# Optimization experiments

Hardware: AMD Instinct MI355X
Metric: run time of the kernel (lower is better)

Reference implementation:

```python
import jax, jax.numpy as jnp
import numpy as np
import math

L, N, D = 1024, 64, 64
O = 1024

def setup_inputs() -> dict:
    key = jax.random.key(0)
    k1, k2 = jax.random.split(key)
    x = jax.random.normal(k1, (L, N, D), dtype=jnp.float32)
    upfold = jax.random.normal(k2, (O, N, D), dtype=jnp.float32)
    return {"x": x, "upfold": upfold}

def reference(x, upfold):
    # x: [L, N, D], upfold: [O, N, D]
    d = x.shape[-1]
    scale = 1.0 / math.sqrt(d)
    # affinities: [L, O, N]
    affinities = jnp.einsum('lnd,ond->lon', x, upfold) * scale
    # weighted sum with (sigmoid - 0.5) weights: [L, N, D]
    features = jnp.einsum('lon,ond->lnd', jax.nn.sigmoid(affinities) - 0.5, upfold)
    return features
```

## Files before the change

### kernel.cpp

```cpp
#include <hip/hip_runtime.h>
#include <stdint.h>

#define L_DIM 1024
#define N_DIM 64
#define D_DIM 64
#define O_DIM 1024
#define ND    4096
#define NT    16

typedef float    floatx16 __attribute__((ext_vector_type(16)));
typedef _Float16 half8    __attribute__((ext_vector_type(8)));
typedef _Float16 h2       __attribute__((ext_vector_type(2)));
typedef __fp16   fp16x2   __attribute__((ext_vector_type(2)));

#define BUF_STRIDE 17920

__device__ __forceinline__ uint32_t pkh2(float a, float b) {
    fp16x2 p = __builtin_amdgcn_cvt_pkrtz(a, b);
    return __builtin_bit_cast(uint32_t, p);
}

__device__ __forceinline__ half8 mk_frag(uint32_t a, uint32_t b, uint32_t c, uint32_t d) {
    union { uint32_t u[4]; half8 v; } U;
    U.u[0] = a; U.u[1] = b; U.u[2] = c; U.u[3] = d;
    return U.v;
}

__device__ __forceinline__ uint32_t psig(float s0, float s1) {
    const h2 HI = {(_Float16)41.6f,        (_Float16)41.6f};
    const h2 LO = {(_Float16)-41.6f,       (_Float16)-41.6f};
    const h2 SC = {(_Float16)0.0625f,      (_Float16)0.0625f};
    const h2 C0 = {(_Float16)0.03099238f,  (_Float16)0.03099238f};
    const h2 C1 = {(_Float16)-0.00842090f, (_Float16)-0.00842090f};
    const h2 C2 = {(_Float16)0.00151845f,  (_Float16)0.00151845f};
    const h2 C3 = {(_Float16)-1.02197e-4f, (_Float16)-1.02197e-4f};
    h2 s = __builtin_bit_cast(h2, pkh2(s0, s1));
    s = __builtin_elementwise_min(s, HI);
    s = __builtin_elementwise_max(s, LO);
    h2 ha = s * SC;
    h2 v  = ha * ha;
    h2 w  = C2 + v * C3;
    w     = C1 + v * w;
    w     = C0 + v * w;
    h2 f  = s * w;
    return __builtin_bit_cast(uint32_t, f);
}

__device__ __forceinline__ void load_tile(const float* ubase, int ot,
                                          int r8, int c, float4* va, float4* vb) {
    const float* pr = ubase + (size_t)(ot * 64 + 2 * r8) * ND + 4 * c;
    #pragma unroll
    for (int j = 0; j < 2; ++j) {
        va[j] = *(const float4*)(pr + (size_t)(32 * j) * ND);
        vb[j] = *(const float4*)(pr + (size_t)(32 * j) * ND + ND);
    }
}

__global__ void __launch_bounds__(256, 2)
corr_kernel(const float* __restrict__ x, const float* __restrict__ up,
            float* __restrict__ out)
{
    __shared__ __align__(16) unsigned char smem[2 * BUF_STRIDE];

    const int tid  = threadIdx.x;
    const int lane = tid & 63;
    const int wid  = tid >> 6;
    const int l31  = lane & 31;
    const int h    = lane >> 5;
    const int r8   = tid >> 4;
    const int c    = tid & 15;
    const int n    = blockIdx.x;
    const int lb   = blockIdx.y;
    const int lw   = lb * 128 + wid * 32 + l31;

    const float* ubase = up + (size_t)n * D_DIM;

    float4 va[2], vb[2];
    load_tile(ubase, 0, r8, c, va, vb);

    half8 Xf[4];
    {
        float (*Xs)[68] = (float (*)[68])smem;
        const int xr = tid >> 1;
        const int xh = tid & 1;
        const float* xsrc = x + (size_t)(lb * 128 + xr) * ND + n * D_DIM;
        #pragma unroll
        for (int j = 0; j < 8; ++j) {
            const int f4i = xh * 8 + j;
            *(float4*)&Xs[xr][4 * f4i] = *(const float4*)(xsrc + 4 * f4i);
        }
        __syncthreads();
        const int rl = wid * 32 + l31;
        #pragma unroll
        for (int kk = 0; kk < 4; ++kk) {
            float4 f1 = *(const float4*)&Xs[rl][16 * kk + 8 * h];
            float4 f2 = *(const float4*)&Xs[rl][16 * kk + 8 * h + 4];
            Xf[kk] = mk_frag(pkh2(f1.x, f1.y), pkh2(f1.z, f1.w),
                             pkh2(f2.x, f2.y), pkh2(f2.z, f2.w));
        }
        __syncthreads();
    }

    #pragma unroll
    for (int j = 0; j < 2; ++j) {
        uint16_t (*Ub)[72]  = (uint16_t (*)[72])(smem);
        uint32_t (*Ut2)[68] = (uint32_t (*)[68])(smem + 9216);
        *(uint2*)&Ub[2*r8 + 32*j][4*c] =
            make_uint2(pkh2(va[j].x, va[j].y), pkh2(va[j].z, va[j].w));
        *(uint2*)&Ub[2*r8 + 32*j + 1][4*c] =
            make_uint2(pkh2(vb[j].x, vb[j].y), pkh2(vb[j].z, vb[j].w));
        *(uint4*)&Ut2[r8 + 16*j][4*c] =
            make_uint4(pkh2(va[j].x, vb[j].x), pkh2(va[j].y, vb[j].y),
                       pkh2(va[j].z, vb[j].z), pkh2(va[j].w, vb[j].w));
    }
    load_tile(ubase, 1, r8, c, va, vb);
    __syncthreads();

    floatx16 F0, F1;
    #pragma unroll
    for (int i = 0; i < 16; ++i) { F0[i] = 0.0f; F1[i] = 0.0f; }

    for (int ot = 0; ot < NT; ++ot) {
        const int b = ot & 1;
        uint16_t (*Ub)[72]   = (uint16_t (*)[72])(smem + b * BUF_STRIDE);
        const uint32_t* utp  = (const uint32_t*)(smem + b * BUF_STRIDE + 9216);
        uint16_t (*Ubn)[72]  = (uint16_t (*)[72])(smem + (b ^ 1) * BUF_STRIDE);
        uint32_t (*Ut2n)[68] = (uint32_t (*)[68])(smem + (b ^ 1) * BUF_STRIDE + 9216);

        half8 A0k[4], A1k[4];
        #pragma unroll
        for (int kk = 0; kk < 4; ++kk) {
            A0k[kk] = *(const half8*)&Ub[l31][16 * kk + 8 * h];
            A1k[kk] = *(const half8*)&Ub[32 + l31][16 * kk + 8 * h];
        }

        if (ot + 1 < NT) {
            #pragma unroll
            for (int j = 0; j < 2; ++j) {
                *(uint2*)&Ubn[2*r8 + 32*j][4*c] =
                    make_uint2(pkh2(va[j].x, va[j].y), pkh2(va[j].z, va[j].w));
                *(uint2*)&Ubn[2*r8 + 32*j + 1][4*c] =
                    make_uint2(pkh2(vb[j].x, vb[j].y), pkh2(vb[j].z, vb[j].w));
                *(uint4*)&Ut2n[r8 + 16*j][4*c] =
                    make_uint4(pkh2(va[j].x, vb[j].x), pkh2(va[j].y, vb[j].y),
                               pkh2(va[j].z, vb[j].z), pkh2(va[j].w, vb[j].w));
            }
        }
        if (ot + 2 < NT)
            load_tile(ubase, ot + 2, r8, c, va, vb);

        floatx16 S0, S1;
        #pragma unroll
        for (int i = 0; i < 16; ++i) { S0[i] = 0.0f; S1[i] = 0.0f; }
        #pragma unroll
        for (int kk = 0; kk < 4; ++kk) {
            S0 = __builtin_amdgcn_mfma_f32_32x32x16_f16(A0k[kk], Xf[kk], S0, 0, 0, 0);
            S1 = __builtin_amdgcn_mfma_f32_32x32x16_f16(A1k[kk], Xf[kk], S1, 0, 0, 0);
        }

        uint32_t P[16];
        #pragma unroll
        for (int m = 0; m < 8; ++m) P[m]     = psig(S0[2*m], S0[2*m+1]);
        #pragma unroll
        for (int m = 0; m < 8; ++m) P[8 + m] = psig(S1[2*m], S1[2*m+1]);

        uint32_t R[8];
        #pragma unroll
        for (int c2 = 0; c2 < 4; ++c2) {
            const uint32_t* Q = P + (c2 >> 1) * 8;
            const int t4 = (c2 & 1) * 4;
            R[2*c2]   = __shfl_xor(h ? Q[t4]     : Q[t4 + 2], 32);
            R[2*c2+1] = __shfl_xor(h ? Q[t4 + 1] : Q[t4 + 3], 32);
        }
        #pragma unroll
        for (int c2 = 0; c2 < 4; ++c2) {
            const uint32_t* Q = P + (c2 >> 1) * 8;
            const int t4 = (c2 & 1) * 4;
            half8 B = h ? mk_frag(R[2*c2], R[2*c2+1], Q[t4 + 2], Q[t4 + 3])
                        : mk_frag(Q[t4], Q[t4 + 1], R[2*c2], R[2*c2+1]);
            const int opb = 8 * c2 + 4 * h;
            uint32_t a0[4], a1[4];
            #pragma unroll
            for (int k = 0; k < 4; ++k) {
                a0[k] = utp[(opb + k) * 68 + l31];
                a1[k] = utp[(opb + k) * 68 + 32 + l31];
            }
            half8 A0 = mk_frag(a0[0], a0[1], a0[2], a0[3]);
            half8 A1 = mk_frag(a1[0], a1[1], a1[2], a1[3]);
            F0 = __builtin_amdgcn_mfma_f32_32x32x16_f16(A0, B, F0, 0, 0, 0);
            F1 = __builtin_amdgcn_mfma_f32_32x32x16_f16(A1, B, F1, 0, 0, 0);
        }
        __syncthreads();
    }

    float* op = out + (size_t)lw * ND + n * D_DIM;
    #pragma unroll
    for (int q = 0; q < 4; ++q) {
        float4 a; a.x = F0[4*q]; a.y = F0[4*q+1]; a.z = F0[4*q+2]; a.w = F0[4*q+3];
        *(float4*)(op + 8*q + 4*h) = a;
        float4 bq; bq.x = F1[4*q]; bq.y = F1[4*q+1]; bq.z = F1[4*q+2]; bq.w = F1[4*q+3];
        *(float4*)(op + 32 + 8*q + 4*h) = bq;
    }
}

extern "C" void kernel_launch(void* const* d_in, const int* in_sizes, int n_in,
                              void* d_out, int out_size, void* d_ws, size_t ws_size,
                              hipStream_t stream)
{
    const float* x  = (const float*)d_in[0];
    const float* up = (const float*)d_in[1];
    float* out      = (float*)d_out;
    dim3 grid(N_DIM, L_DIM / 128);
    corr_kernel<<<grid, dim3(256), 0, stream>>>(x, up, out);
}
```

Before: 101.2 us.

## Precompute fp16 upfold layouts in a prepass and stream them via direct global-to-LDS loads

A new prepass kernel converts upfold to fp16 once, writing both a row-major and a transposed layout into workspace. The main kernel then stages tiles straight into LDS with global_load_lds and XOR-swizzled addressing, so it no longer does per-tile fp32 loads, conversion and LDS writes in registers. Each of the eight L-blocks previously repeated that conversion for the same n. The cost is a second kernel launch and an extra workspace round trip through global memory, and the prefetch of the next tile now overlaps the current tile's compute without a register-held copy.

```diff
diff --git a/kernel.cpp b/kernel.cpp
--- a/kernel.cpp
+++ b/kernel.cpp
@@ -1,19 +1,16 @@
 #include <hip/hip_runtime.h>
 #include <stdint.h>
 
-#define L_DIM 1024
-#define N_DIM 64
-#define D_DIM 64
-#define O_DIM 1024
-#define ND    4096
-#define NT    16
+#define ND       4096
+#define NT       16
+#define A_OFF    0
+#define B_OFF    8388608
+#define N_STRIDE 131072
 
 typedef float    floatx16 __attribute__((ext_vector_type(16)));
 typedef _Float16 half8    __attribute__((ext_vector_type(8)));
 typedef _Float16 h2       __attribute__((ext_vector_type(2)));
 typedef __fp16   fp16x2   __attribute__((ext_vector_type(2)));
-
-#define BUF_STRIDE 17920
 
 __device__ __forceinline__ uint32_t pkh2(float a, float b) {
     fp16x2 p = __builtin_amdgcn_cvt_pkrtz(a, b);
@@ -46,44 +43,81 @@
     return __builtin_bit_cast(uint32_t, f);
 }
 
-__device__ __forceinline__ void load_tile(const float* ubase, int ot,
-                                          int r8, int c, float4* va, float4* vb) {
-    const float* pr = ubase + (size_t)(ot * 64 + 2 * r8) * ND + 4 * c;
+__device__ __forceinline__ void gl_lds16(const void* g, void* l) {
+    __builtin_amdgcn_global_load_lds(
+        (const __attribute__((address_space(1))) unsigned int*)g,
+        (__attribute__((address_space(3))) unsigned int*)l, 16, 0, 0);
+}
+
+__global__ void __launch_bounds__(256, 4)
+conv_kernel(const float* __restrict__ up, uint8_t* __restrict__ ws)
+{
+    const int tid = threadIdx.x;
+    const int n   = blockIdx.x;
+    const int oq  = blockIdx.y;
+    const int r8  = tid >> 4;
+    const int c   = tid & 15;
+    const float* pr = up + (size_t)(oq * 64 + 2 * r8) * ND + n * 64 + 4 * c;
+    uint8_t* An = ws + A_OFF + (size_t)n * N_STRIDE;
+    uint8_t* Bn = ws + B_OFF + (size_t)n * N_STRIDE;
     #pragma unroll
     for (int j = 0; j < 2; ++j) {
-        va[j] = *(const float4*)(pr + (size_t)(32 * j) * ND);
-        vb[j] = *(const float4*)(pr + (size_t)(32 * j) * ND + ND);
+        float4 fa = *(const float4*)(pr + (size_t)(32 * j) * ND);
+        float4 fb = *(const float4*)(pr + (size_t)(32 * j) * ND + ND);
+        const int o0 = oq * 64 + 2 * r8 + 32 * j;
+        *(uint2*)(An + (size_t)o0 * 128 + 8 * c) =
+            make_uint2(pkh2(fa.x, fa.y), pkh2(fa.z, fa.w));
+        *(uint2*)(An + (size_t)(o0 + 1) * 128 + 8 * c) =
+            make_uint2(pkh2(fb.x, fb.y), pkh2(fb.z, fb.w));
+        const float av[4] = {fa.x, fa.y, fa.z, fa.w};
+        const float bv[4] = {fb.x, fb.y, fb.z, fb.w};
+        #pragma unroll
+        for (int k = 0; k < 4; ++k)
+            *(uint32_t*)(Bn + (size_t)(4 * c + k) * 2048 + 2 * o0) = pkh2(av[k], bv[k]);
     }
 }
 
 __global__ void __launch_bounds__(256, 2)
-corr_kernel(const float* __restrict__ x, const float* __restrict__ up,
+corr_kernel(const float* __restrict__ x, const uint8_t* __restrict__ ws,
             float* __restrict__ out)
 {
-    __shared__ __align__(16) unsigned char smem[2 * BUF_STRIDE];
+    __shared__ __align__(16) uint8_t smem[2][16384];
+    __shared__ __align__(16) float Xs[128][68];
 
     const int tid  = threadIdx.x;
     const int lane = tid & 63;
     const int wid  = tid >> 6;
     const int l31  = lane & 31;
     const int h    = lane >> 5;
-    const int r8   = tid >> 4;
-    const int c    = tid & 15;
     const int n    = blockIdx.x;
     const int lb   = blockIdx.y;
     const int lw   = lb * 128 + wid * 32 + l31;
 
-    const float* ubase = up + (size_t)n * D_DIM;
-
-    float4 va[2], vb[2];
-    load_tile(ubase, 0, r8, c, va, vb);
+    const int ric = lane >> 3;
+    const int gsw = (lane & 7) ^ ric;
+    const uint32_t voffA = ric * 128  + gsw * 16;
+    const uint32_t voffB = ric * 2048 + gsw * 16;
+    const uint8_t* An = ws + A_OFF + (size_t)n * N_STRIDE;
+    const uint8_t* Bn = ws + B_OFF + (size_t)n * N_STRIDE;
+    const int q0 = 2 * wid, q1 = q0 + 1;
+
+    auto stage = [&](int ot, int b) {
+        const uint8_t* At = An + ot * 8192;
+        const uint8_t* Bt = Bn + ot * 128;
+        uint8_t* L = &smem[b][0];
+        gl_lds16(At + q0 * 1024  + voffA, L + q0 * 1024);
+        gl_lds16(At + q1 * 1024  + voffA, L + q1 * 1024);
+        gl_lds16(Bt + q0 * 16384 + voffB, L + 8192 + q0 * 1024);
+        gl_lds16(Bt + q1 * 16384 + voffB, L + 8192 + q1 * 1024);
+    };
+
+    stage(0, 0);
 
     half8 Xf[4];
     {
-        float (*Xs)[68] = (float (*)[68])smem;
         const int xr = tid >> 1;
         const int xh = tid & 1;
-        const float* xsrc = x + (size_t)(lb * 128 + xr) * ND + n * D_DIM;
+        const float* xsrc = x + (size_t)(lb * 128 + xr) * ND + n * 64;
         #pragma unroll
         for (int j = 0; j < 8; ++j) {
             const int f4i = xh * 8 + j;
@@ -98,56 +132,33 @@
             Xf[kk] = mk_frag(pkh2(f1.x, f1.y), pkh2(f1.z, f1.w),
                              pkh2(f2.x, f2.y), pkh2(f2.z, f2.w));
         }
-        __syncthreads();
-    }
-
-    #pragma unroll
-    for (int j = 0; j < 2; ++j) {
-        uint16_t (*Ub)[72]  = (uint16_t (*)[72])(smem);
-        uint32_t (*Ut2)[68] = (uint32_t (*)[68])(smem + 9216);
-        *(uint2*)&Ub[2*r8 + 32*j][4*c] =
-            make_uint2(pkh2(va[j].x, va[j].y), pkh2(va[j].z, va[j].w));
-        *(uint2*)&Ub[2*r8 + 32*j + 1][4*c] =
-            make_uint2(pkh2(vb[j].x, vb[j].y), pkh2(vb[j].z, vb[j].w));
-        *(uint4*)&Ut2[r8 + 16*j][4*c] =
-            make_uint4(pkh2(va[j].x, vb[j].x), pkh2(va[j].y, vb[j].y),
-                       pkh2(va[j].z, vb[j].z), pkh2(va[j].w, vb[j].w));
-    }
-    load_tile(ubase, 1, r8, c, va, vb);
-    __syncthreads();
+    }
 
     floatx16 F0, F1;
     #pragma unroll
     for (int i = 0; i < 16; ++i) { F0[i] = 0.0f; F1[i] = 0.0f; }
 
+    const int sw = l31 & 7;
+
     for (int ot = 0; ot < NT; ++ot) {
         const int b = ot & 1;
-        uint16_t (*Ub)[72]   = (uint16_t (*)[72])(smem + b * BUF_STRIDE);
-        const uint32_t* utp  = (const uint32_t*)(smem + b * BUF_STRIDE + 9216);
-        uint16_t (*Ubn)[72]  = (uint16_t (*)[72])(smem + (b ^ 1) * BUF_STRIDE);
-        uint32_t (*Ut2n)[68] = (uint32_t (*)[68])(smem + (b ^ 1) * BUF_STRIDE + 9216);
+        if (ot + 1 < NT) stage(ot + 1, b ^ 1);
+        const uint8_t* L = &smem[b][0];
 
         half8 A0k[4], A1k[4];
         #pragma unroll
         for (int kk = 0; kk < 4; ++kk) {
-            A0k[kk] = *(const half8*)&Ub[l31][16 * kk + 8 * h];
-            A1k[kk] = *(const half8*)&Ub[32 + l31][16 * kk + 8 * h];
-        }
-
-        if (ot + 1 < NT) {
-            #pragma unroll
-            for (int j = 0; j < 2; ++j) {
-                *(uint2*)&Ubn[2*r8 + 32*j][4*c] =
-                    make_uint2(pkh2(va[j].x, va[j].y), pkh2(va[j].z, va[j].w));
-                *(uint2*)&Ubn[2*r8 + 32*j + 1][4*c] =
-                    make_uint2(pkh2(vb[j].x, vb[j].y), pkh2(vb[j].z, vb[j].w));
-                *(uint4*)&Ut2n[r8 + 16*j][4*c] =
-                    make_uint4(pkh2(va[j].x, vb[j].x), pkh2(va[j].y, vb[j].y),
-                               pkh2(va[j].z, vb[j].z), pkh2(va[j].w, vb[j].w));
-            }
-        }
-        if (ot + 2 < NT)
-            load_tile(ubase, ot + 2, r8, c, va, vb);
+            const int bi = ((2 * kk + h) ^ sw) * 16;
+            A0k[kk] = *(const half8*)(L + l31 * 128 + bi);
+            A1k[kk] = *(const half8*)(L + (32 + l31) * 128 + bi);
+        }
+        half8 B0k[4], B1k[4];
+        #pragma unroll
+        for (int c2 = 0; c2 < 4; ++c2) {
+            const int bi = ((2 * c2 + h) ^ sw) * 16;
+            B0k[c2] = *(const half8*)(L + 8192 + l31 * 128 + bi);
+            B1k[c2] = *(const half8*)(L + 8192 + (32 + l31) * 128 + bi);
+        }
 
         floatx16 S0, S1;
         #pragma unroll
@@ -178,22 +189,13 @@
             const int t4 = (c2 & 1) * 4;
             half8 B = h ? mk_frag(R[2*c2], R[2*c2+1], Q[t4 + 2], Q[t4 + 3])
                         : mk_frag(Q[t4], Q[t4 + 1], R[2*c2], R[2*c2+1]);
-            const int opb = 8 * c2 + 4 * h;
-            uint32_t a0[4], a1[4];
-            #pragma unroll
-            for (int k = 0; k < 4; ++k) {
-                a0[k] = utp[(opb + k) * 68 + l31];
-                a1[k] = utp[(opb + k) * 68 + 32 + l31];
-            }
-            half8 A0 = mk_frag(a0[0], a0[1], a0[2], a0[3]);
-            half8 A1 = mk_frag(a1[0], a1[1], a1[2], a1[3]);
-            F0 = __builtin_amdgcn_mfma_f32_32x32x16_f16(A0, B, F0, 0, 0, 0);
-            F1 = __builtin_amdgcn_mfma_f32_32x32x16_f16(A1, B, F1, 0, 0, 0);
+            F0 = __builtin_amdgcn_mfma_f32_32x32x16_f16(B0k[c2], B, F0, 0, 0, 0);
+            F1 = __builtin_amdgcn_mfma_f32_32x32x16_f16(B1k[c2], B, F1, 0, 0, 0);
         }
         __syncthreads();
     }
 
-    float* op = out + (size_t)lw * ND + n * D_DIM;
+    float* op = out + (size_t)lw * ND + n * 64;
     #pragma unroll
     for (int q = 0; q < 4; ++q) {
         float4 a; a.x = F0[4*q]; a.y = F0[4*q+1]; a.z = F0[4*q+2]; a.w = F0[4*q+3];
@@ -210,6 +212,7 @@
     const float* x  = (const float*)d_in[0];
     const float* up = (const float*)d_in[1];
     float* out      = (float*)d_out;
-    dim3 grid(N_DIM, L_DIM / 128);
-    corr_kernel<<<grid, dim3(256), 0, stream>>>(x, up, out);
-}
+    uint8_t* ws     = (uint8_t*)d_ws;
+    conv_kernel<<<dim3(64, 16), dim3(256), 0, stream>>>(up, ws);
+    corr_kernel<<<dim3(64, 8),  dim3(256), 0, stream>>>(x, ws, out);
+}
```

Result: slower. 110.7 us (+9.4%).
